# Optimization experiments

Hardware: AMD Instinct MI355X
Metric: run time of the kernel (lower is better)

Reference implementation:

```python
import jax, jax.numpy as jnp
import numpy as np

D_K = 128
NEG_MAX = float(np.finfo(np.float32).max)  # original uses -finfo(float32).max


def setup_inputs() -> dict:
    key = jax.random.key(0)
    kq, kk, kv, km = jax.random.split(key, 4)
    B, S, D = 16, 2048, D_K
    q = jax.random.normal(kq, (B, S, D), dtype=jnp.float32)
    k = jax.random.normal(kk, (B, S, D), dtype=jnp.float32)
    v = jax.random.normal(kv, (B, S, D), dtype=jnp.float32)
    mask = jax.random.randint(km, (B, S, S), 0, 2).astype(jnp.bool_)
    return {"q": q, "k": k, "v": v, "mask": mask}


def reference(q, k, v, mask):
    # scores: [B, S, S] = q @ k^T / sqrt(d_k)
    scale = 1.0 / np.sqrt(D_K).astype(np.float32)
    scores = jnp.einsum('bqd,bkd->bqk', q, k) * scale
    scores = jnp.where(mask, -NEG_MAX, scores)  # masked_fill with -float32 max
    attn = jax.nn.softmax(scores, axis=2)
    return jnp.einsum('bqk,bkd->bqd', attn, v)
```

## Files before the change

### kernel.cpp

```cpp
#include <hip/hip_runtime.h>

#define NTHREADS 256

typedef __attribute__((ext_vector_type(8))) short bf16x8;
typedef __attribute__((ext_vector_type(4))) float f32x4;
typedef __attribute__((ext_vector_type(2))) unsigned uint2v;
typedef __attribute__((ext_vector_type(4))) unsigned uint4v;

constexpr int kB = 16, kS = 2048, kD = 128;
constexpr int QBLK = 64, KBLK = 64;
constexpr int MSTRIDE = 68;
constexpr float kNegMax = -3.402823466e38f;
constexpr float kMClamp = -1e30f;

__device__ __forceinline__ unsigned cvt_pk(float lo, float hi) {
    unsigned r;
    asm("v_cvt_pk_bf16_f32 %0, %1, %2" : "=v"(r) : "v"(lo), "v"(hi));
    return r;
}

#define SWZ(bytecol, row) ((bytecol) ^ (((row) & 7) << 4))
#define SWZV(bytecol, row) ((bytecol) ^ (((((row) & 7) ^ (((row) >> 2) & 7)) & 7) << 4))
#define SWZP(bytecol, row) ((bytecol) ^ (((row) & 7) << 4))

template<int SPLIT>
__global__ __launch_bounds__(NTHREADS, 2)
void attn_fwd(const float* __restrict__ q, const float* __restrict__ k,
              const float* __restrict__ v, const int* __restrict__ mask,
              float* __restrict__ out, float* __restrict__ ws)
{
    __shared__ __align__(16) char smem[45312];
    char* K_lds  = smem;
    char* VT_lds = smem + 16384;
    char* P_lds  = smem + 32768;
    unsigned char* M_lds = (unsigned char*)(smem + 40960);

    const int tid = threadIdx.x, lane = tid & 63, w = tid >> 6;
    const int l15 = lane & 15, lg = lane >> 4;

    const int bid = (int)blockIdx.x;
    int b, qbase, kbase;
    if (SPLIT == 1) {
        int swz = (bid & 7) * 64 + (bid >> 3);
        b = swz >> 5; qbase = (swz & 31) * QBLK; kbase = 0;
    } else {
        int swz = (bid & 7) * 128 + (bid >> 3);
        b = swz >> 6;
        int rem = swz & 63;
        qbase = (rem >> 1) * QBLK;
        kbase = (rem & 1) * (kS / 2);
    }
    const int nrounds = (SPLIT == 1) ? (kS / KBLK) : (kS / KBLK / 2);

    const float scale = 0.08838834764831845f;
    bf16x8 qf[4];
    {
        const float* qp = q + ((size_t)(b*kS + qbase + w*16 + l15)) * kD;
        #pragma unroll
        for (int kk = 0; kk < 4; ++kk) {
            float4 a = *(const float4*)(qp + kk*32 + lg*8);
            float4 c = *(const float4*)(qp + kk*32 + lg*8 + 4);
            uint4v pk = { cvt_pk(a.x*scale, a.y*scale), cvt_pk(a.z*scale, a.w*scale),
                          cvt_pk(c.x*scale, c.y*scale), cvt_pk(c.z*scale, c.w*scale) };
            qf[kk] = __builtin_bit_cast(bf16x8, pk);
        }
    }

    f32x4 acc[8];
    #pragma unroll
    for (int d = 0; d < 8; ++d) acc[d] = f32x4{0.f,0.f,0.f,0.f};
    float m_r = kMClamp, l_r = 0.f;

    const float* kbat = k + (size_t)b * kS * kD;
    const float* vbat = v + (size_t)b * kS * kD;
    const int*   mbat = mask + ((size_t)b * kS + qbase) * kS;

    char* Pw = P_lds + w * 2048;

    float4 kreg[4][2];
    float4 vreg[2][4];
    int4   mreg[4];

    auto LOAD = [&](int kt0) {
        #pragma unroll
        for (int c = 0; c < 4; ++c) {
            int chunk = c * 256 + tid;
            int row = chunk >> 4, col8 = chunk & 15;
            const float4* ptr = (const float4*)(kbat + (size_t)(kt0 + row)*kD + col8*8);
            kreg[c][0] = ptr[0];
            kreg[c][1] = ptr[1];
        }
        #pragma unroll
        for (int it = 0; it < 2; ++it) {
            int blk = it * 256 + tid;
            int kg = blk >> 5, dg = blk & 31;
            #pragma unroll
            for (int r = 0; r < 4; ++r)
                vreg[it][r] = *(const float4*)(vbat + (size_t)(kt0 + kg*4 + r)*kD + dg*4);
        }
        #pragma unroll
        for (int c = 0; c < 4; ++c) {
            int idx = c * 256 + tid;
            int mrow = idx >> 4, mc4 = idx & 15;
            mreg[c] = *(const int4*)(mbat + (size_t)mrow*kS + kt0 + mc4*4);
        }
    };

    auto STORE = [&]() {
        #pragma unroll
        for (int c = 0; c < 4; ++c) {
            int chunk = c * 256 + tid;
            int row = chunk >> 4, col8 = chunk & 15;
            uint4v pk = { cvt_pk(kreg[c][0].x, kreg[c][0].y), cvt_pk(kreg[c][0].z, kreg[c][0].w),
                          cvt_pk(kreg[c][1].x, kreg[c][1].y), cvt_pk(kreg[c][1].z, kreg[c][1].w) };
            *(uint4v*)(K_lds + row*256 + SWZ(col8*16, row)) = pk;
        }
        #pragma unroll
        for (int it = 0; it < 2; ++it) {
            int blk = it * 256 + tid;
            int kg = blk >> 5, dg = blk & 31;
            #pragma unroll
            for (int jj = 0; jj < 4; ++jj) {
                int row = dg * 4 + jj;
                uint2v pk = { cvt_pk((&vreg[it][0].x)[jj], (&vreg[it][1].x)[jj]),
                              cvt_pk((&vreg[it][2].x)[jj], (&vreg[it][3].x)[jj]) };
                *(uint2v*)(VT_lds + row*128 + SWZV(kg*8, row)) = pk;
            }
        }
        #pragma unroll
        for (int c = 0; c < 4; ++c) {
            int idx = c * 256 + tid;
            int mrow = idx >> 4, mc4 = idx & 15;
            unsigned pk = (unsigned)(mreg[c].x != 0)
                        | ((unsigned)(mreg[c].y != 0) << 8)
                        | ((unsigned)(mreg[c].z != 0) << 16)
                        | ((unsigned)(mreg[c].w != 0) << 24);
            *(unsigned*)(M_lds + mrow*MSTRIDE + mc4*4) = pk;
        }
    };

    LOAD(kbase);

    for (int t = 0; t < nrounds; ++t) {
        __syncthreads();
        STORE();
        __syncthreads();
        if (t + 1 < nrounds) LOAD(kbase + (t + 1) * KBLK);

        f32x4 z[4];
        #pragma unroll
        for (int kt = 0; kt < 4; ++kt) {
            f32x4 zz = f32x4{0.f,0.f,0.f,0.f};
            int krow = kt*16 + l15;
            #pragma unroll
            for (int kk = 0; kk < 4; ++kk) {
                bf16x8 kf = *(const bf16x8*)(K_lds + krow*256 + SWZ(kk*64 + lg*16, krow));
                zz = __builtin_amdgcn_mfma_f32_16x16x32_bf16(kf, qf[kk], zz, 0, 0, 0);
            }
            z[kt] = zz;
        }

        const int mrowb = (w*16 + l15) * MSTRIDE;
        float mx = kNegMax;
        #pragma unroll
        for (int kt = 0; kt < 4; ++kt) {
            unsigned nib = *(const unsigned*)(M_lds + mrowb + kt*16 + lg*4);
            #pragma unroll
            for (int i = 0; i < 4; ++i) {
                float sv = ((nib >> (8*i)) & 0xFFu) ? kNegMax : z[kt][i];
                z[kt][i] = sv;
                mx = fmaxf(mx, sv);
            }
        }
        mx = fmaxf(mx, __shfl_xor(mx, 16));
        mx = fmaxf(mx, __shfl_xor(mx, 32));
        float mnew = fmaxf(m_r, mx);
        float corr = __expf(m_r - mnew);
        float rs = 0.f;
        #pragma unroll
        for (int kt = 0; kt < 4; ++kt) {
            float p0 = __expf(z[kt][0] - mnew);
            float p1 = __expf(z[kt][1] - mnew);
            float p2 = __expf(z[kt][2] - mnew);
            float p3 = __expf(z[kt][3] - mnew);
            rs += (p0 + p1) + (p2 + p3);
            uint2v pk = { cvt_pk(p0, p1), cvt_pk(p2, p3) };
            *(uint2v*)(Pw + l15*128 + SWZP(kt*32 + lg*8, l15)) = pk;
        }
        rs += __shfl_xor(rs, 16);
        rs += __shfl_xor(rs, 32);
        m_r = mnew;
        l_r = l_r * corr + rs;
        #pragma unroll
        for (int d = 0; d < 8; ++d) acc[d] *= corr;

        #pragma unroll
        for (int ks = 0; ks < 2; ++ks) {
            bf16x8 pf = *(const bf16x8*)(Pw + l15*128 + SWZP(ks*64 + lg*16, l15));
            #pragma unroll
            for (int dblk = 0; dblk < 8; ++dblk) {
                int vrow = dblk*16 + l15;
                bf16x8 vf = *(const bf16x8*)(VT_lds + vrow*128 + SWZV(ks*64 + lg*16, vrow));
                acc[dblk] = __builtin_amdgcn_mfma_f32_16x16x32_bf16(vf, pf, acc[dblk], 0, 0, 0);
            }
        }
    }

    if (SPLIT == 1) {
        float inv = 1.0f / l_r;
        float* op = out + ((size_t)(b*kS + qbase + w*16 + l15)) * kD;
        #pragma unroll
        for (int dblk = 0; dblk < 8; ++dblk) {
            float4 r;
            r.x = acc[dblk][0] * inv;
            r.y = acc[dblk][1] * inv;
            r.z = acc[dblk][2] * inv;
            r.w = acc[dblk][3] * inv;
            *(float4*)(op + dblk*16 + lg*4) = r;
        }
    } else {
        const int half = (kbase != 0);
        const size_t row = (size_t)half * (kB*kS) + (size_t)b*kS + qbase + w*16 + l15;
        float* op = ws + row * kD;
        #pragma unroll
        for (int dblk = 0; dblk < 8; ++dblk) {
            float4 r;
            r.x = acc[dblk][0]; r.y = acc[dblk][1];
            r.z = acc[dblk][2]; r.w = acc[dblk][3];
            *(float4*)(op + dblk*16 + lg*4) = r;
        }
        if (lg == 0) {
            float* ml = ws + (size_t)2*kB*kS*kD;
            ml[row*2 + 0] = m_r;
            ml[row*2 + 1] = l_r;
        }
    }
}

__global__ __launch_bounds__(NTHREADS)
void attn_merge(const float* __restrict__ ws, float* __restrict__ out)
{
    const float* ml = ws + (size_t)2*kB*kS*kD;
    const int tid = threadIdx.x;
    const size_t r = (size_t)blockIdx.x * 8 + (tid >> 5);
    const int c = (tid & 31) * 4;
    float m0 = ml[r*2 + 0],               l0 = ml[r*2 + 1];
    float m1 = ml[((size_t)kB*kS + r)*2], l1 = ml[((size_t)kB*kS + r)*2 + 1];
    float mS = fmaxf(m0, m1);
    float e0 = __expf(m0 - mS), e1 = __expf(m1 - mS);
    float inv = 1.0f / (l0*e0 + l1*e1);
    float4 o0 = *(const float4*)(ws + r*kD + c);
    float4 o1 = *(const float4*)(ws + (size_t)kB*kS*kD + r*kD + c);
    float4 rr;
    rr.x = (o0.x*e0 + o1.x*e1) * inv;
    rr.y = (o0.y*e0 + o1.y*e1) * inv;
    rr.z = (o0.z*e0 + o1.z*e1) * inv;
    rr.w = (o0.w*e0 + o1.w*e1) * inv;
    *(float4*)(out + r*kD + c) = rr;
}

extern "C" void kernel_launch(void* const* d_in, const int* in_sizes, int n_in,
                              void* d_out, int out_size, void* d_ws, size_t ws_size,
                              hipStream_t stream) {
    const float* q = (const float*)d_in[0];
    const float* k = (const float*)d_in[1];
    const float* v = (const float*)d_in[2];
    const int* mask = (const int*)d_in[3];
    float* out = (float*)d_out;
    const size_t wsNeeded = (size_t)2*kB*kS*kD*4 + (size_t)2*kB*kS*2*4;
    if (ws_size >= wsNeeded) {
        attn_fwd<2><<<dim3(kB * (kS/QBLK) * 2), dim3(NTHREADS), 0, stream>>>(
            q, k, v, mask, out, (float*)d_ws);
        attn_merge<<<dim3(kB*kS/8), dim3(NTHREADS), 0, stream>>>((const float*)d_ws, out);
    } else {
        attn_fwd<1><<<dim3(kB * (kS/QBLK)), dim3(NTHREADS), 0, stream>>>(
            q, k, v, mask, out, nullptr);
    }
}
```

Measured before the change: 120.6 us.

## Halve key block to 32 and raise occupancy to four blocks per CU

Result: slower. 126.8 us (+5.2%).

```diff
diff --git a/kernel.cpp b/kernel.cpp
--- a/kernel.cpp
+++ b/kernel.cpp
@@ -8,8 +8,8 @@
 typedef __attribute__((ext_vector_type(4))) unsigned uint4v;
 
 constexpr int kB = 16, kS = 2048, kD = 128;
-constexpr int QBLK = 64, KBLK = 64;
-constexpr int MSTRIDE = 68;
+constexpr int QBLK = 64, KBLK = 32;
+constexpr int MSTRIDE = 36;
 constexpr float kNegMax = -3.402823466e38f;
 constexpr float kMClamp = -1e30f;
 
@@ -20,20 +20,20 @@
 }
 
 #define SWZ(bytecol, row) ((bytecol) ^ (((row) & 7) << 4))
-#define SWZV(bytecol, row) ((bytecol) ^ (((((row) & 7) ^ (((row) >> 2) & 7)) & 7) << 4))
-#define SWZP(bytecol, row) ((bytecol) ^ (((row) & 7) << 4))
+#define SWZV2(bytecol, row) ((bytecol) ^ ((((row) >> 2) & 3) << 4))
+#define SWZP2(bytecol, row) ((bytecol) ^ (((row) & 3) << 4))
 
 template<int SPLIT>
-__global__ __launch_bounds__(NTHREADS, 2)
+__global__ __launch_bounds__(NTHREADS, 4)
 void attn_fwd(const float* __restrict__ q, const float* __restrict__ k,
               const float* __restrict__ v, const int* __restrict__ mask,
               float* __restrict__ out, float* __restrict__ ws)
 {
-    __shared__ __align__(16) char smem[45312];
+    __shared__ __align__(16) char smem[22784];
     char* K_lds  = smem;
-    char* VT_lds = smem + 16384;
-    char* P_lds  = smem + 32768;
-    unsigned char* M_lds = (unsigned char*)(smem + 40960);
+    char* VT_lds = smem + 8192;
+    char* P_lds  = smem + 16384;
+    unsigned char* M_lds = (unsigned char*)(smem + 20480);
 
     const int tid = threadIdx.x, lane = tid & 63, w = tid >> 6;
     const int l15 = lane & 15, lg = lane >> 4;
@@ -75,15 +75,16 @@
     const float* vbat = v + (size_t)b * kS * kD;
     const int*   mbat = mask + ((size_t)b * kS + qbase) * kS;
 
-    char* Pw = P_lds + w * 2048;
-
-    float4 kreg[4][2];
-    float4 vreg[2][4];
-    int4   mreg[4];
+    char* Pw = P_lds + w * 1024;
+    const int kg = tid >> 5, dg = tid & 31;
+
+    float4 kreg[2][2];
+    float4 vreg[4];
+    int4   mreg[2];
 
     auto LOAD = [&](int kt0) {
         #pragma unroll
-        for (int c = 0; c < 4; ++c) {
+        for (int c = 0; c < 2; ++c) {
             int chunk = c * 256 + tid;
             int row = chunk >> 4, col8 = chunk & 15;
             const float4* ptr = (const float4*)(kbat + (size_t)(kt0 + row)*kD + col8*8);
@@ -91,24 +92,19 @@
             kreg[c][1] = ptr[1];
         }
         #pragma unroll
-        for (int it = 0; it < 2; ++it) {
-            int blk = it * 256 + tid;
-            int kg = blk >> 5, dg = blk & 31;
-            #pragma unroll
-            for (int r = 0; r < 4; ++r)
-                vreg[it][r] = *(const float4*)(vbat + (size_t)(kt0 + kg*4 + r)*kD + dg*4);
-        }
-        #pragma unroll
-        for (int c = 0; c < 4; ++c) {
+        for (int r = 0; r < 4; ++r)
+            vreg[r] = *(const float4*)(vbat + (size_t)(kt0 + kg*4 + r)*kD + dg*4);
+        #pragma unroll
+        for (int c = 0; c < 2; ++c) {
             int idx = c * 256 + tid;
-            int mrow = idx >> 4, mc4 = idx & 15;
+            int mrow = idx >> 3, mc4 = idx & 7;
             mreg[c] = *(const int4*)(mbat + (size_t)mrow*kS + kt0 + mc4*4);
         }
     };
 
     auto STORE = [&]() {
         #pragma unroll
-        for (int c = 0; c < 4; ++c) {
+        for (int c = 0; c < 2; ++c) {
             int chunk = c * 256 + tid;
             int row = chunk >> 4, col8 = chunk & 15;
             uint4v pk = { cvt_pk(kreg[c][0].x, kreg[c][0].y), cvt_pk(kreg[c][0].z, kreg[c][0].w),
@@ -116,21 +112,16 @@
             *(uint4v*)(K_lds + row*256 + SWZ(col8*16, row)) = pk;
         }
         #pragma unroll
-        for (int it = 0; it < 2; ++it) {
-            int blk = it * 256 + tid;
-            int kg = blk >> 5, dg = blk & 31;
-            #pragma unroll
-            for (int jj = 0; jj < 4; ++jj) {
-                int row = dg * 4 + jj;
-                uint2v pk = { cvt_pk((&vreg[it][0].x)[jj], (&vreg[it][1].x)[jj]),
-                              cvt_pk((&vreg[it][2].x)[jj], (&vreg[it][3].x)[jj]) };
-                *(uint2v*)(VT_lds + row*128 + SWZV(kg*8, row)) = pk;
-            }
-        }
-        #pragma unroll
-        for (int c = 0; c < 4; ++c) {
+        for (int jj = 0; jj < 4; ++jj) {
+            int row = dg * 4 + jj;
+            uint2v pk = { cvt_pk((&vreg[0].x)[jj], (&vreg[1].x)[jj]),
+                          cvt_pk((&vreg[2].x)[jj], (&vreg[3].x)[jj]) };
+            *(uint2v*)(VT_lds + row*64 + SWZV2(kg*8, row)) = pk;
+        }
+        #pragma unroll
+        for (int c = 0; c < 2; ++c) {
             int idx = c * 256 + tid;
-            int mrow = idx >> 4, mc4 = idx & 15;
+            int mrow = idx >> 3, mc4 = idx & 7;
             unsigned pk = (unsigned)(mreg[c].x != 0)
                         | ((unsigned)(mreg[c].y != 0) << 8)
                         | ((unsigned)(mreg[c].z != 0) << 16)
@@ -147,9 +138,9 @@
         __syncthreads();
         if (t + 1 < nrounds) LOAD(kbase + (t + 1) * KBLK);
 
-        f32x4 z[4];
-        #pragma unroll
-        for (int kt = 0; kt < 4; ++kt) {
+        f32x4 z[2];
+        #pragma unroll
+        for (int kt = 0; kt < 2; ++kt) {
             f32x4 zz = f32x4{0.f,0.f,0.f,0.f};
             int krow = kt*16 + l15;
             #pragma unroll
@@ -163,7 +154,7 @@
         const int mrowb = (w*16 + l15) * MSTRIDE;
         float mx = kNegMax;
         #pragma unroll
-        for (int kt = 0; kt < 4; ++kt) {
+        for (int kt = 0; kt < 2; ++kt) {
             unsigned nib = *(const unsigned*)(M_lds + mrowb + kt*16 + lg*4);
             #pragma unroll
             for (int i = 0; i < 4; ++i) {
@@ -178,14 +169,14 @@
         float corr = __expf(m_r - mnew);
         float rs = 0.f;
         #pragma unroll
-        for (int kt = 0; kt < 4; ++kt) {
+        for (int kt = 0; kt < 2; ++kt) {
             float p0 = __expf(z[kt][0] - mnew);
             float p1 = __expf(z[kt][1] - mnew);
             float p2 = __expf(z[kt][2] - mnew);
             float p3 = __expf(z[kt][3] - mnew);
             rs += (p0 + p1) + (p2 + p3);
             uint2v pk = { cvt_pk(p0, p1), cvt_pk(p2, p3) };
-            *(uint2v*)(Pw + l15*128 + SWZP(kt*32 + lg*8, l15)) = pk;
+            *(uint2v*)(Pw + l15*64 + SWZP2(kt*32 + lg*8, l15)) = pk;
         }
         rs += __shfl_xor(rs, 16);
         rs += __shfl_xor(rs, 32);
@@ -194,15 +185,12 @@
         #pragma unroll
         for (int d = 0; d < 8; ++d) acc[d] *= corr;
 
-        #pragma unroll
-        for (int ks = 0; ks < 2; ++ks) {
-            bf16x8 pf = *(const bf16x8*)(Pw + l15*128 + SWZP(ks*64 + lg*16, l15));
-            #pragma unroll
-            for (int dblk = 0; dblk < 8; ++dblk) {
-                int vrow = dblk*16 + l15;
-                bf16x8 vf = *(const bf16x8*)(VT_lds + vrow*128 + SWZV(ks*64 + lg*16, vrow));
-                acc[dblk] = __builtin_amdgcn_mfma_f32_16x16x32_bf16(vf, pf, acc[dblk], 0, 0, 0);
-            }
+        bf16x8 pf = *(const bf16x8*)(Pw + l15*64 + SWZP2(lg*16, l15));
+        #pragma unroll
+        for (int dblk = 0; dblk < 8; ++dblk) {
+            int vrow = dblk*16 + l15;
+            bf16x8 vf = *(const bf16x8*)(VT_lds + vrow*64 + SWZV2(lg*16, vrow));
+            acc[dblk] = __builtin_amdgcn_mfma_f32_16x16x32_bf16(vf, pf, acc[dblk], 0, 0, 0);
         }
     }
 
```
